# Kernel optimization log

Hardware: AMD Instinct MI355X
Metric: run time of the kernel (lower is better)

## Reference

```python
import jax, jax.numpy as jnp
import numpy as np

B = 4; C = 3; IMG = 256; P = 16; HP = 16; HW = 256
DIM = 512; DEPTH = 6; HEADS = 8; DH = 64
NS = 50; SH = 4; SDH = 64; ITERS = 3; RPD = 128; FF = 2048; N = NS + HW


def _ln(x, g, b):
    m = jnp.mean(x, -1, keepdims=True)
    v = jnp.var(x, -1, keepdims=True)
    return (x - m) * jax.lax.rsqrt(v + 1e-5) * g + b


def _rms(x, g):
    # lucidrains RMSNorm: F.normalize(x, dim=-1) * sqrt(dim) * gamma
    n = jnp.linalg.norm(x, axis=-1, keepdims=True)
    return x / jnp.maximum(n, 1e-12) * (DIM ** 0.5) * g


def setup_inputs() -> dict:
    key = jax.random.key(0)
    ks = iter(jax.random.split(key, 64))
    def W(*s):
        return jax.random.normal(next(ks), s, jnp.float32) * 0.02
    SI = SH * SDH
    d = {}
    d['images'] = jax.random.normal(next(ks), (B, C, IMG, IMG), jnp.float32)
    d['slot_noise'] = jax.random.normal(next(ks), (B, NS, DIM), jnp.float32)
    d['patch_w'] = W(C * P * P, DIM); d['patch_b'] = jnp.zeros((DIM,))
    d['hpos'] = W(HP, DIM); d['wpos'] = W(HP, DIM)
    d['rp_w1'] = W(2, RPD); d['rp_b1'] = jnp.zeros((RPD,))
    d['rp_w2'] = W(RPD, RPD); d['rp_b2'] = jnp.zeros((RPD,))
    d['rp_w3'] = W(RPD, HEADS); d['rp_b3'] = jnp.zeros((HEADS,))
    d['slots_mu'] = W(1, 1, DIM); d['slots_logsigma'] = jnp.zeros((1, 1, DIM))
    d['sa_ln_in_g'] = jnp.ones((DIM,)); d['sa_ln_in_b'] = jnp.zeros((DIM,))
    d['sa_ln_sl_g'] = jnp.ones((DIM,)); d['sa_ln_sl_b'] = jnp.zeros((DIM,))
    d['sa_wq'] = W(DIM, SI); d['sa_bq'] = jnp.zeros((SI,))
    d['sa_wk'] = W(DIM, SI); d['sa_bk'] = jnp.zeros((SI,))
    d['sa_wv'] = W(DIM, SI); d['sa_bv'] = jnp.zeros((SI,))
    d['sa_wo'] = W(SI, DIM); d['sa_bo'] = jnp.zeros((DIM,))
    d['gru_wih'] = W(DIM, 3 * DIM); d['gru_whh'] = W(DIM, 3 * DIM)
    d['gru_bih'] = jnp.zeros((3 * DIM,)); d['gru_bhh'] = jnp.zeros((3 * DIM,))
    d['sa_ln_ff_g'] = jnp.ones((DIM,)); d['sa_ln_ff_b'] = jnp.zeros((DIM,))
    d['sa_mlp_w1'] = W(DIM, DIM); d['sa_mlp_b1'] = jnp.zeros((DIM,))
    d['sa_mlp_w2'] = W(DIM, DIM); d['sa_mlp_b2'] = jnp.zeros((DIM,))
    d['s2c_w'] = W(DIM, 2); d['s2c_b'] = jnp.zeros((2,))
    d['attn_g'] = jnp.ones((DEPTH, DIM))
    d['wq'] = W(DEPTH, DIM, HEADS * DH); d['wk'] = W(DEPTH, DIM, HEADS * DH)
    d['wv'] = W(DEPTH, DIM, HEADS * DH); d['wo'] = W(DEPTH, HEADS * DH, DIM)
    d['ff_g'] = jnp.ones((DEPTH, DIM))
    d['ff_w1'] = W(DEPTH, DIM, FF); d['ff_b1'] = jnp.zeros((DEPTH, FF))
    d['ff_w2'] = W(DEPTH, FF, DIM); d['ff_b2'] = jnp.zeros((DEPTH, DIM))
    d['final_g'] = jnp.ones((DIM,))
    d['pred_w'] = W(DIM, DIM); d['pred_b'] = jnp.zeros((DIM,))
    return d


def reference(images, slot_noise, patch_w, patch_b, hpos, wpos,
              rp_w1, rp_b1, rp_w2, rp_b2, rp_w3, rp_b3,
              slots_mu, slots_logsigma, sa_ln_in_g, sa_ln_in_b, sa_ln_sl_g, sa_ln_sl_b,
              sa_wq, sa_bq, sa_wk, sa_bk, sa_wv, sa_bv, sa_wo, sa_bo,
              gru_wih, gru_whh, gru_bih, gru_bhh, sa_ln_ff_g, sa_ln_ff_b,
              sa_mlp_w1, sa_mlp_b1, sa_mlp_w2, sa_mlp_b2, s2c_w, s2c_b,
              attn_g, wq, wk, wv, wo, ff_g, ff_w1, ff_b1, ff_w2, ff_b2,
              final_g, pred_w, pred_b):
    b = images.shape[0]
    # patchify: b c (h p1) (w p2) -> b h w (p1 p2 c)
    x = images.reshape(b, C, HP, P, HP, P).transpose(0, 2, 4, 3, 5, 1).reshape(b, HP, HP, P * P * C)
    tokens = x @ patch_w + patch_b                     # [b, HP, HP, DIM]
    tokens = tokens + hpos[:, None, :] + wpos[None, :, :]
    tokens = tokens.reshape(b, HW, DIM)
    # --- multi-head slot attention ---
    inp = _ln(tokens, sa_ln_in_g, sa_ln_in_b)
    k = (inp @ sa_wk + sa_bk).reshape(b, HW, SH, SDH).transpose(0, 2, 1, 3)
    v = (inp @ sa_wv + sa_bv).reshape(b, HW, SH, SDH).transpose(0, 2, 1, 3)
    slots = slots_mu + jnp.exp(slots_logsigma) * slot_noise  # [b, NS, DIM]
    scale = SDH ** -0.5
    for _ in range(ITERS):
        prev = slots
        s = _ln(slots, sa_ln_sl_g, sa_ln_sl_b)
        q = (s @ sa_wq + sa_bq).reshape(b, NS, SH, SDH).transpose(0, 2, 1, 3)
        dots = jnp.einsum('bhid,bhjd->bhij', q, k) * scale     # [b, SH, NS, HW]
        attn = jax.nn.softmax(dots, axis=-2) + 1e-8            # softmax over slots
        attn = attn / jnp.sum(attn, -1, keepdims=True)         # weighted mean over inputs
        upd = jnp.einsum('bhij,bhjd->bhid', attn, v)
        upd = upd.transpose(0, 2, 1, 3).reshape(b, NS, SH * SDH) @ sa_wo + sa_bo
        # GRUCell(updates, prev_slots)
        gx = upd @ gru_wih + gru_bih
        gh = prev @ gru_whh + gru_bhh
        xr, xz, xn = jnp.split(gx, 3, -1)
        hr, hz, hn = jnp.split(gh, 3, -1)
        r = jax.nn.sigmoid(xr + hr)
        z = jax.nn.sigmoid(xz + hz)
        nn_ = jnp.tanh(xn + r * hn)
        slots = (1 - z) * nn_ + z * prev
        slots = slots + (jax.nn.relu(_ln(slots, sa_ln_ff_g, sa_ln_ff_b) @ sa_mlp_w1 + sa_mlp_b1) @ sa_mlp_w2 + sa_mlp_b2)
    objects = slots
    slot_coords = objects @ s2c_w + s2c_b              # [b, NS, 2]
    # --- relative position MLP bias (slots coords + patch grid) ---
    g = jnp.arange(HP, dtype=jnp.float32)
    grid = jnp.stack(jnp.meshgrid(g, g, indexing='ij'), -1).reshape(HW, 2)
    coords = jnp.concatenate([slot_coords, jnp.broadcast_to(grid, (b, HW, 2))], axis=1)  # [b, N, 2]
    rel = coords[:, :, None, :] - coords[:, None, :, :]   # [b, N, N, 2]
    hmid = jax.nn.silu(rel @ rp_w1 + rp_b1)
    hmid = jax.nn.silu(hmid @ rp_w2 + rp_b2)
    bias = jnp.transpose(hmid @ rp_w3 + rp_b3, (0, 3, 1, 2))  # [b, HEADS, N, N]
    # --- transformer with per-layer rel-pos bias ---
    x = jnp.concatenate([objects, tokens], axis=1)     # [b, N, DIM]
    ascale = DH ** -0.5
    for l in range(DEPTH):
        h = _rms(x, attn_g[l])
        qh = (h @ wq[l]).reshape(b, N, HEADS, DH).transpose(0, 2, 1, 3)
        kh = (h @ wk[l]).reshape(b, N, HEADS, DH).transpose(0, 2, 1, 3)
        vh = (h @ wv[l]).reshape(b, N, HEADS, DH).transpose(0, 2, 1, 3)
        sim = jnp.einsum('bhid,bhjd->bhij', qh, kh) * ascale + bias
        a = jax.nn.softmax(sim, -1)
        o = jnp.einsum('bhij,bhjd->bhid', a, vh).transpose(0, 2, 1, 3).reshape(b, N, HEADS * DH) @ wo[l]
        x = x + o
        h = _rms(x, ff_g[l])
        x = x + (jax.nn.gelu(h @ ff_w1[l] + ff_b1[l]) @ ff_w2[l] + ff_b2[l])
    x = _rms(x, final_g)
    return x[:, NS:] @ pred_w + pred_b                 # [b, HW, DIM]
```

## Files before the change

### kernel.cpp

```cpp
#include <hip/hip_runtime.h>
#include <hip/hip_bf16.h>

typedef __hip_bfloat16 bf16;
typedef short short8v __attribute__((ext_vector_type(8)));
typedef float float4v __attribute__((ext_vector_type(4)));

static __device__ __forceinline__ float b2f(bf16 x){ return __bfloat162float(x); }

static __device__ __forceinline__ float ldin(const void* p, size_t i, bool isbf) {
  return isbf ? b2f(((const bf16*)p)[i]) : ((const float*)p)[i];
}

static __device__ __forceinline__ unsigned short f2bu(float f) {
  bf16 h = __float2bfloat16(f);
  return *reinterpret_cast<unsigned short*>(&h);
}

#define CDIV(a,b) (((a)+(b)-1)/(b))

#define NB   4
#define NSL  50
#define HWT  256
#define NT   306
#define DIM  512
// ... 104 lines not shown
  for (int k0 = kbeg; k0 < kend; k0 += 32) {
    *(short8v*)&As[srow * LDT + sch] = *(short8v*)ha;
    *(short8v*)&Bs[srow * LDT + sch] = *(short8v*)hb;
    __syncthreads();
    if (k0 + 32 < kend) { fetchA(k0 + 32); fetchB(k0 + 32); }
    short8v a0 = *reinterpret_cast<const short8v*>(&As[(wm + ti)      * LDT + quad * 8]);
    short8v a1 = *reinterpret_cast<const short8v*>(&As[(wm + 16 + ti) * LDT + quad * 8]);
    short8v b0 = *reinterpret_cast<const short8v*>(&Bs[(wn + ti)      * LDT + quad * 8]);
    short8v b1 = *reinterpret_cast<const short8v*>(&Bs[(wn + 16 + ti) * LDT + quad * 8]);
    acc00 = __builtin_amdgcn_mfma_f32_16x16x32_bf16(a0, b0, acc00, 0, 0, 0);
    acc01 = __builtin_amdgcn_mfma_f32_16x16x32_bf16(a0, b1, acc01, 0, 0, 0);
    acc10 = __builtin_amdgcn_mfma_f32_16x16x32_bf16(a1, b0, acc10, 0, 0, 0);
    acc11 = __builtin_amdgcn_mfma_f32_16x16x32_bf16(a1, b1, acc11, 0, 0, 0);
    __syncthreads();
  }

  float4v accs[2][2] = {{acc00, acc01}, {acc10, acc11}};
#pragma unroll
  for (int mi = 0; mi < 2; ++mi) {
#pragma unroll
    for (int ni = 0; ni < 2; ++ni) {
      int row0 = bm + wm + mi * 16 + quad * 4;
      int col  = bn + wn + ni * 16 + ti;
      float bv = (bias && kbeg == 0) ? ldin(bias, boff + col, isbf) : 0.f;
#pragma unroll
      for (int r = 0; r < 4; ++r) {
        int row = row0 + r;
        if (row >= M) continue;
        float v = accs[mi][ni][r] + bv;
        if (act == 1) v = fmaxf(v, 0.f);
        else if (act == 2) {
          float u = 0.7978845608028654f * (v + 0.044715f * v * v * v);
          v = 0.5f * v * (1.f + tanhf(u));
        } else if (act == 3) {
          v = v / (1.f + expf(-v));
        }
        size_t idx = (size_t)row * N + col;
        if (oty) ((bf16*)C)[idx] = __float2bfloat16(v);
        else {
          float* Cf = (float*)C;
          if (mode == 2) atomicAdd(&Cf[idx], v);
          else if (mode == 1) Cf[idx] += v;
          else Cf[idx] = v;
        }
      }
    }
  }
}

__global__ __launch_bounds__(256) void gemm_mfma(
    const void* A, int aty, const unsigned short* WT, size_t woff,
    const void* bias, size_t boff, void* C, int oty,
    int M, int N, int K, int act, int accum, int zsplit, const int* __restrict__ flagp)
{
  int ksz = K / zsplit;
  int kbeg = blockIdx.z * ksz;
  int mode = zsplit > 1 ? 2 : (accum ? 1 : 0);
  gemm_body2(A, aty, WT + woff, bias, boff, C, oty, M, N, K, kbeg, kbeg + ksz,
             act, mode, *flagp != 0);
}

__global__ __launch_bounds__(256) void gemm_mfma_tri(
    const void* A, int aty, const unsigned short* WT, size_t o0, size_t o1, size_t o2,
    void* C0, void* C1, void* C2, int oty, int M, int N, int K,
    const int* __restrict__ flagp)
{
  size_t o = blockIdx.z == 0 ? o0 : (blockIdx.z == 1 ? o1 : o2);
  void* C = blockIdx.z == 0 ? C0 : (blockIdx.z == 1 ? C1 : C2);
  gemm_body2(A, aty, WT + o, nullptr, 0, C, oty, M, N, K, 0, K, 0, 0, *flagp != 0);
}

__global__ __launch_bounds__(256) void gemm_mfma_duo(
    const void* A0, const void* A1, int aty, const unsigned short* WT, size_t o0, size_t o1,
    const void* bias0, const void* bias1, void* C0, void* C1, int oty,
    int M, int N, int K, const int* __restrict__ flagp)
{
  const void* A = blockIdx.z ? A1 : A0;
  size_t o = blockIdx.z ? o1 : o0;
  const void* bias = blockIdx.z ? bias1 : bias0;
  void* C = blockIdx.z ? C1 : C0;
  gemm_body2(A, aty, WT + o, bias, 0, C, oty, M, N, K, 0, K, 0, 0, *flagp != 0);
}

__global__ __launch_bounds__(256) void gemm_k(
    const float* __restrict__ A, const void* __restrict__ W, size_t woff,
    const void* __restrict__ bias, size_t boff, float* __restrict__ C,
    int M, int N, int K, const int* __restrict__ flagp)
{
  const bool isbf = *flagp != 0;
  __shared__ float As[16][68];
  __shared__ float Ws[16][68];
  const int bm = blockIdx.y * 64, bn = blockIdx.x * 64;
  const int tx = threadIdx.x, ty = threadIdx.y;
  const int tid = ty * 16 + tx;
  float acc[4][4] = {};
  for (int k0 = 0; k0 < K; k0 += 16) {
#pragma unroll
    for (int i = 0; i < 4; ++i) {
      int idx = tid + i * 256;
      int m  = idx >> 4, k = idx & 15;
      int gm = bm + m;
      As[k][m] = (gm < M) ? A[(size_t)gm * K + k0 + k] : 0.f;
      int kk = idx >> 6, n = idx & 63;
      int gn = bn + n;
      Ws[kk][n] = (gn < N) ? ldin(W, woff + (size_t)(k0 + kk) * N + gn, isbf) : 0.f;
    }
    __syncthreads();
#pragma unroll
    for (int k = 0; k < 16; ++k) {
      float4 a4 = *reinterpret_cast<const float4*>(&As[k][ty * 4]);
      float4 w4 = *reinterpret_cast<const float4*>(&Ws[k][tx * 4]);
      float a[4] = {a4.x, a4.y, a4.z, a4.w};
      float w[4] = {w4.x, w4.y, w4.z, w4.w};
#pragma unroll
      for (int i = 0; i < 4; ++i)
#pragma unroll
        for (int j = 0; j < 4; ++j)
          acc[i][j] = fmaf(a[i], w[j], acc[i][j]);
    }
    __syncthreads();
  }
#pragma unroll
  for (int i = 0; i < 4; ++i) {
    int gm = bm + ty * 4 + i;
    if (gm >= M) continue;
#pragma unroll
    for (int j = 0; j < 4; ++j) {
      int gn = bn + tx * 4 + j;
      if (gn >= N) continue;
      float v = acc[i][j];
      if (bias) v += ldin(bias, boff + gn, isbf);
      C[(size_t)gm * N + gn] = v;
    }
  }
}

__global__ void patchify_k(const void* __restrict__ img, unsigned short* __restrict__ xp,
                           const int* __restrict__ flagp) {
  const bool isbf = *flagp != 0;
  int i = blockIdx.x * 256 + threadIdx.x;
  if (i >= NB * HWT * 768) return;
  int col = i % 768, row = i / 768;
  int c = col % 3, p2 = (col / 3) & 15, p1 = col / 48;
  int w = row & 15, h = (row >> 4) & 15, b = row >> 8;
  xp[i] = f2bu(ldin(img, (((size_t)(b * 3 + c) * 256 + h * 16 + p1) * 256) + w * 16 + p2, isbf));
}

__global__ void addpos_k(float* __restrict__ tok, const void* __restrict__ hp,
                         const void* __restrict__ wp, const int* __restrict__ flagp) {
  const bool isbf = *flagp != 0;
  int i = blockIdx.x * 256 + threadIdx.x;
  if (i >= NB * HWT * DIM) return;
  int d = i & 511;
  int row = i >> 9;
  int w = row & 15, h = (row >> 4) & 15;
  tok[i] += ldin(hp, h * DIM + d, isbf) + ldin(wp, w * DIM + d, isbf);
}

__global__ void ln512_k(const float* __restrict__ X, const void* __restrict__ g,
                        const void* __restrict__ b, unsigned short* __restrict__ Y,
                        const int* __restrict__ flagp) {
  const bool isbf = *flagp != 0;
  int row = blockIdx.x, t = threadIdx.x;
  const float* x = X + (size_t)row * DIM;
  float v0 = x[t], v1 = x[t + 256];
  __shared__ float rs[256], rq[256];
  rs[t] = v0 + v1; rq[t] = v0 * v0 + v1 * v1;
  __syncthreads();
  for (int o = 128; o > 0; o >>= 1) {
    if (t < o) { rs[t] += rs[t + o]; rq[t] += rq[t + o]; }
    __syncthreads();
  }
  float mean = rs[0] * (1.f / 512.f);
  float var  = rq[0] * (1.f / 512.f) - mean * mean;
  float inv  = rsqrtf(var + 1e-5f);
  unsigned short* y = Y + (size_t)row * DIM;
  y[t]       = f2bu((v0 - mean) * inv * ldin(g, t, isbf)       + ldin(b, t, isbf));
  y[t + 256] = f2bu((v1 - mean) * inv * ldin(g, t + 256, isbf) + ldin(b, t + 256, isbf));
}

__global__ void rms512_k(const float* __restrict__ X, const void* __restrict__ g,
                         int goff, unsigned short* __restrict__ Y, const int* __restrict__ flagp) {
  const bool isbf = *flagp != 0;
  int row = blockIdx.x, t = threadIdx.x;
  const float* x = X + (size_t)row * DIM;
  float v0 = x[t], v1 = x[t + 256];
  __shared__ float rq[256];
  rq[t] = v0 * v0 + v1 * v1;
  __syncthreads();
  for (int o = 128; o > 0; o >>= 1) {
    if (t < o) rq[t] += rq[t + o];
    __syncthreads();
  }
  float nrm = sqrtf(rq[0]);
  float sc = 22.62741699796952f / fmaxf(nrm, 1e-12f);
  unsigned short* y = Y + (size_t)row * DIM;
  y[t]       = f2bu(v0 * sc * ldin(g, goff + t, isbf));
  y[t + 256] = f2bu(v1 * sc * ldin(g, goff + t + 256, isbf));
}

__global__ void slots_init_k(const void* __restrict__ mu, const void* __restrict__ ls,
                             const void* __restrict__ noise, float* __restrict__ slots,
                             const int* __restrict__ flagp) {
  const bool isbf = *flagp != 0;
  int i = blockIdx.x * 256 + threadIdx.x;
  if (i >= NB * NSL * DIM) return;
  int d = i & 511;
  slots[i] = ldin(mu, d, isbf) + expf(ldin(ls, d, isbf)) * ldin(noise, i, isbf);
}

__global__ void slot_dots_k(const float* __restrict__ q, const float* __restrict__ k,
                            float* __restrict__ dots) {
  int blk = blockIdx.x;
  int i = blk % 50, h = (blk / 50) & 3, b = blk / 200;
  int j = threadIdx.x;
  __shared__ float qs[64];
// ... 72 lines not shown
__global__ void relpos_table_k(const void* w1, const void* b1, const void* w2,
                               const void* b2, const void* w3, const void* b3,
                               float* __restrict__ tab, const int* __restrict__ flagp) {
  const bool isbf = *flagp != 0;
  int blk = blockIdx.x;
  float r0 = (float)(blk / 31 - 15), r1 = (float)(blk % 31 - 15);
  int t = threadIdx.x;
  __shared__ float h1[128], h2[128];
  float a = fmaf(r0, ldin(w1, t, isbf), fmaf(r1, ldin(w1, 128 + t, isbf), ldin(b1, t, isbf)));
  h1[t] = a / (1.f + expf(-a));
  __syncthreads();
  float s = ldin(b2, t, isbf);
#pragma unroll 4
  for (int k = 0; k < 128; ++k) s = fmaf(h1[k], ldin(w2, k * 128 + t, isbf), s);
  h2[t] = s / (1.f + expf(-s));
  __syncthreads();
  if (t < 8) {
    float o = ldin(b3, t, isbf);
#pragma unroll 4
    for (int k = 0; k < 128; ++k) o = fmaf(h2[k], ldin(w3, k * 8 + t, isbf), o);
    tab[blk * 8 + t] = o;
  }
}

__global__ void bias_fill_k(const float* __restrict__ tab, float* __restrict__ bias) {
  int i = blockIdx.x * 256 + threadIdx.x;
  if (i >= NB * NH * HWT * HWT) return;
  int jj = i & 255, ii = (i >> 8) & 255, h = (i >> 16) & 7, b = i >> 19;
  int di = (ii >> 4) - (jj >> 4) + 15;
  int dj = (ii & 15) - (jj & 15) + 15;
  bias[(((size_t)(b * NH + h) * NT) + NSL + ii) * NT + NSL + jj] = tab[(di * 31 + dj) * 8 + h];
}

__global__ void rp_l1_k(const float* __restrict__ coords, const void* w1, const void* b1,
                        unsigned short* __restrict__ H, int pbase, int pcount,
                        const int* __restrict__ flagp) {
  const bool isbf = *flagp != 0;
  int idx = blockIdx.x * 256 + threadIdx.x;
  if (idx >= pcount * 128) return;
  int pl = idx >> 7, u = idx & 127;
  int p = pbase + pl;
  int q = p % RPP, bb = p / RPP;
  int ii, jj;
  rp_decode(q, ii, jj);
  float r0 = coords[(bb * NT + ii) * 2]     - coords[(bb * NT + jj) * 2];
  float r1 = coords[(bb * NT + ii) * 2 + 1] - coords[(bb * NT + jj) * 2 + 1];
  float a = fmaf(r0, ldin(w1, u, isbf), fmaf(r1, ldin(w1, 128 + u, isbf), ldin(b1, u, isbf)));
  H[(size_t)pl * 128 + u] = f2bu(a / (1.f + expf(-a)));
}

__global__ __launch_bounds__(256) void rp_l3_k(
    const unsigned short* __restrict__ H2, const void* w3, const void* b3,
    float* __restrict__ bias, int pbase, int pcount, const int* __restrict__ flagp) {
  const bool isbf = *flagp != 0;
  __shared__ float W3s[128 * 8];
  int t = threadIdx.x;
  for (int e = t; e < 1024; e += 256) W3s[e] = ldin(w3, e, isbf);
  __syncthreads();
  int pl = blockIdx.x * 32 + (t >> 3), hh = t & 7;
  if (pl >= pcount) return;
  int p = pbase + pl;
  int q = p % RPP, bb = p / RPP;
  int ii, jj;
  rp_decode(q, ii, jj);
  float s = ldin(b3, hh, isbf);
  const unsigned short* hrow = H2 + (size_t)pl * 128;
#pragma unroll 8
  for (int k = 0; k < 128; ++k) {
    bf16 hv = *reinterpret_cast<const bf16*>(&hrow[k]);
    s = fmaf(b2f(hv), W3s[k * 8 + hh], s);
  }
  bias[((size_t)(bb * NH + hh) * NT + ii) * NT + jj] = s;
}

__global__ void build_x_k(const float* __restrict__ slots, const float* __restrict__ tok,
                          float* __restrict__ x) {
  int i = blockIdx.x * 256 + threadIdx.x;
  if (i >= NB * NT * DIM) return;
  int d = i & 511, n = (i >> 9) % NT, b = i / (NT * DIM);
  x[i] = (n < NSL) ? slots[((size_t)(b * NSL + n)) * DIM + d]
                   : tok[((size_t)(b * HWT + (n - NSL))) * DIM + d];
}

__global__ __launch_bounds__(256) void attn_sim_k(
    const unsigned short* __restrict__ Qb, const unsigned short* __restrict__ Kb,
    const float* __restrict__ bias, float* __restrict__ sim)
{
  const int bh = blockIdx.z, b = bh >> 3, h = bh & 7;
  const int bm = blockIdx.y * 64, bn = blockIdx.x * 64;
  __shared__ unsigned short As[64 * 72];
  __shared__ unsigned short Bs[64 * 72];
  const int tid = threadIdx.x;
  const int lane = tid & 63, wave = tid >> 6, quad = lane >> 4, ti = lane & 15;
  const int wm = (wave & 1) * 32, wn = (wave >> 1) * 32;
  {
    int r = tid >> 2, c = (tid & 3) * 16;
    ushort4 z4 = {0,0,0,0};
    ushort4 a[4] = {z4, z4, z4, z4}, bq[4] = {z4, z4, z4, z4};
    int gi = bm + r, gj = bn + r;
    if (gi < NT) {
      const ushort4* p = reinterpret_cast<const ushort4*>(Qb + ((size_t)(b * NT + gi)) * DIM + h * 64 + c);
#pragma unroll
      for (int i = 0; i < 4; ++i) a[i] = p[i];
    }
    if (gj < NT) {
      const ushort4* p = reinterpret_cast<const ushort4*>(Kb + ((size_t)(b * NT + gj)) * DIM + h * 64 + c);
#pragma unroll
      for (int i = 0; i < 4; ++i) bq[i] = p[i];
    }
#pragma unroll
    for (int i = 0; i < 4; ++i) {
      *reinterpret_cast<ushort4*>(&As[r * 72 + c + i * 4]) = a[i];
      *reinterpret_cast<ushort4*>(&Bs[r * 72 + c + i * 4]) = bq[i];
    }
  }
  __syncthreads();
  float4v acc00 = {0,0,0,0}, acc01 = {0,0,0,0}, acc10 = {0,0,0,0}, acc11 = {0,0,0,0};
#pragma unroll
  for (int ks = 0; ks < 2; ++ks) {
    short8v a0 = *reinterpret_cast<const short8v*>(&As[(wm + ti)      * 72 + ks * 32 + quad * 8]);
    short8v a1 = *reinterpret_cast<const short8v*>(&As[(wm + 16 + ti) * 72 + ks * 32 + quad * 8]);
    short8v b0 = *reinterpret_cast<const short8v*>(&Bs[(wn + ti)      * 72 + ks * 32 + quad * 8]);
    short8v b1 = *reinterpret_cast<const short8v*>(&Bs[(wn + 16 + ti) * 72 + ks * 32 + quad * 8]);
    acc00 = __builtin_amdgcn_mfma_f32_16x16x32_bf16(a0, b0, acc00, 0, 0, 0);
    acc01 = __builtin_amdgcn_mfma_f32_16x16x32_bf16(a0, b1, acc01, 0, 0, 0);
    acc10 = __builtin_amdgcn_mfma_f32_16x16x32_bf16(a1, b0, acc10, 0, 0, 0);
    acc11 = __builtin_amdgcn_mfma_f32_16x16x32_bf16(a1, b1, acc11, 0, 0, 0);
  }
  float4v accs[2][2] = {{acc00, acc01}, {acc10, acc11}};
#pragma unroll
  for (int mi = 0; mi < 2; ++mi) {
#pragma unroll
    for (int ni = 0; ni < 2; ++ni) {
      int row0 = bm + wm + mi * 16 + quad * 4;
      int col  = bn + wn + ni * 16 + ti;
      if (col >= NT) continue;
#pragma unroll
      for (int r = 0; r < 4; ++r) {
        int row = row0 + r;
        if (row >= NT) continue;
        size_t idx = ((size_t)bh * NT + row) * NT + col;
        sim[idx] = accs[mi][ni][r] * 0.125f + bias[idx];
      }
    }
  }
}

__global__ void softmax_prob_k(const float* __restrict__ sim, unsigned short* __restrict__ prob) {
  int row = blockIdx.x;
  const float* src = sim + (size_t)row * NT;
  unsigned short* dst = prob + (size_t)row * 320;
  int t = threadIdx.x;
  float v0 = (t < NT) ? src[t] : -1e30f;
  float v1 = (t + 256 < NT) ? src[t + 256] : -1e30f;
  __shared__ float rb[256];
  rb[t] = fmaxf(v0, v1);
  __syncthreads();
  for (int o = 128; o > 0; o >>= 1) {
    if (t < o) rb[t] = fmaxf(rb[t], rb[t + o]);
    __syncthreads();
  }
  float m = rb[0];
  __syncthreads();
  float e0 = (t < NT) ? expf(v0 - m) : 0.f;
  float e1 = (t + 256 < NT) ? expf(v1 - m) : 0.f;
  rb[t] = e0 + e1;
  __syncthreads();
  for (int o = 128; o > 0; o >>= 1) {
    if (t < o) rb[t] += rb[t + o];
    __syncthreads();
  }
  float inv = 1.f / rb[0];
  dst[t] = f2bu(e0 * inv);
  if (t + 256 < 320) dst[t + 256] = f2bu(t + 256 < NT ? e1 * inv : 0.f);
}

__global__ __launch_bounds__(256) void attn_av_k(
    const unsigned short* __restrict__ prob, const unsigned short* __restrict__ Vb,
    unsigned short* __restrict__ Ob)
{
  const int bh = blockIdx.y, b = bh >> 3, h = bh & 7;
  const int bm = blockIdx.x * 64;
  __shared__ unsigned short As[64 * LDT];
  __shared__ unsigned short Bs[64 * LDT];
  const int tid = threadIdx.x;
  const int lane = tid & 63, wave = tid >> 6, quad = lane >> 4, ti = lane & 15;
  const int wm = (wave & 1) * 32, wn = (wave >> 1) * 32;
  const int arow = tid >> 2, ach = (tid & 3) * 8;
  const int bk = tid & 31, bch = tid >> 5;

  float4v acc00 = {0,0,0,0}, acc01 = {0,0,0,0}, acc10 = {0,0,0,0}, acc11 = {0,0,0,0};

  for (int k0 = 0; k0 < 320; k0 += 32) {
    {
      int gi = bm + arow;
      ushort4 u0 = {0,0,0,0}, u1 = {0,0,0,0};
      if (gi < NT) {
        const ushort4* p = reinterpret_cast<const ushort4*>(
            prob + ((size_t)bh * NT + gi) * 320 + k0 + ach);
        u0 = p[0]; u1 = p[1];
      }
      *reinterpret_cast<ushort4*>(&As[arow * LDT + ach])     = u0;
      *reinterpret_cast<ushort4*>(&As[arow * LDT + ach + 4]) = u1;
    }
    {
      int j = k0 + bk;
      unsigned short h8[8];
      if (j < NT) {
        const ushort4* p = reinterpret_cast<const ushort4*>(
            Vb + ((size_t)(b * NT + j)) * DIM + h * 64 + bch * 8);
        ushort4 u0 = p[0], u1 = p[1];
        h8[0]=u0.x; h8[1]=u0.y; h8[2]=u0.z; h8[3]=u0.w; h8[4]=u1.x; h8[5]=u1.y; h8[6]=u1.z; h8[7]=u1.w;
      } else {
#pragma unroll
        for (int i = 0; i < 8; ++i) h8[i] = 0;
      }
#pragma unroll
      for (int i = 0; i < 8; ++i) Bs[(bch * 8 + i) * LDT + bk] = h8[i];
    }
    __syncthreads();
    short8v a0 = *reinterpret_cast<const short8v*>(&As[(wm + ti)      * LDT + quad * 8]);
    short8v a1 = *reinterpret_cast<const short8v*>(&As[(wm + 16 + ti) * LDT + quad * 8]);
    short8v b0 = *reinterpret_cast<const short8v*>(&Bs[(wn + ti)      * LDT + quad * 8]);
    short8v b1 = *reinterpret_cast<const short8v*>(&Bs[(wn + 16 + ti) * LDT + quad * 8]);
    acc00 = __builtin_amdgcn_mfma_f32_16x16x32_bf16(a0, b0, acc00, 0, 0, 0);
    acc01 = __builtin_amdgcn_mfma_f32_16x16x32_bf16(a0, b1, acc01, 0, 0, 0);
    acc10 = __builtin_amdgcn_mfma_f32_16x16x32_bf16(a1, b0, acc10, 0, 0, 0);
    acc11 = __builtin_amdgcn_mfma_f32_16x16x32_bf16(a1, b1, acc11, 0, 0, 0);
    __syncthreads();
  }
  float4v accs[2][2] = {{acc00, acc01}, {acc10, acc11}};
#pragma unroll
  for (int mi = 0; mi < 2; ++mi) {
#pragma unroll
    for (int ni = 0; ni < 2; ++ni) {
      int row0 = bm + wm + mi * 16 + quad * 4;
      int col  = wn + ni * 16 + ti;
#pragma unroll
      for (int r = 0; r < 4; ++r) {
        int row = row0 + r;
        if (row >= NT) continue;
        Ob[((size_t)(b * NT + row)) * DIM + h * 64 + col] = f2bu(accs[mi][ni][r]);
      }
    }
  }
}

__global__ void write_out_k(const float* __restrict__ tmp, void* __restrict__ out,
                            const int* __restrict__ flagp) {
  const bool isbf = *flagp != 0;
  int i = blockIdx.x * 256 + threadIdx.x;
  if (i >= NB * HWT * DIM) return;
  int d = i & 511, tt = (i >> 9) & 255, b = i / (HWT * DIM);
  float v = tmp[((size_t)(b * NT + NSL + tt)) * DIM + d];
  if (isbf) ((bf16*)out)[i] = __float2bfloat16(v);
  else      ((float*)out)[i] = v;
}

extern "C" void kernel_launch(void* const* d_in, const int* in_sizes, int n_in,
                              void* d_out, int out_size, void* d_ws, size_t ws_size,
                              hipStream_t stream) {
  const void* images        = d_in[0];
  const void* slot_noise    = d_in[1];
  const void* patch_w       = d_in[2];
  const void* patch_b       = d_in[3];
  const void* hpos          = d_in[4];
  const void* wpos          = d_in[5];
  const void* rp_w1         = d_in[6];
  const void* rp_b1         = d_in[7];
  const void* rp_w2         = d_in[8];
  const void* rp_b2         = d_in[9];
  const void* rp_w3         = d_in[10];
  const void* rp_b3         = d_in[11];
  const void* slots_mu      = d_in[12];
  const void* slots_logsig  = d_in[13];
  const void* sa_ln_in_g    = d_in[14];
  const void* sa_ln_in_b    = d_in[15];
  const void* sa_ln_sl_g    = d_in[16];
  const void* sa_ln_sl_b    = d_in[17];
  const void* sa_wq         = d_in[18];
  const void* sa_bq         = d_in[19];
  const void* sa_wk         = d_in[20];
  const void* sa_bk         = d_in[21];
  const void* sa_wv         = d_in[22];
  const void* sa_bv         = d_in[23];
  const void* sa_wo         = d_in[24];
  const void* sa_bo         = d_in[25];
  const void* gru_wih       = d_in[26];
  const void* gru_whh       = d_in[27];
  const void* gru_bih       = d_in[28];
  const void* gru_bhh       = d_in[29];
  const void* sa_ln_ff_g    = d_in[30];
  const void* sa_ln_ff_b    = d_in[31];
  const void* sa_mlp_w1     = d_in[32];
  const void* sa_mlp_b1     = d_in[33];
  const void* sa_mlp_w2     = d_in[34];
  const void* sa_mlp_b2     = d_in[35];
  const void* s2c_w         = d_in[36];
  const void* s2c_b         = d_in[37];
  const void* attn_g        = d_in[38];
  const void* wq            = d_in[39];
  const void* wk            = d_in[40];
  const void* wv            = d_in[41];
  const void* wo            = d_in[42];
  const void* ff_g          = d_in[43];
  const void* ff_w1         = d_in[44];
  const void* ff_b1         = d_in[45];
  const void* ff_w2         = d_in[46];
  const void* ff_b2         = d_in[47];
  const void* final_g       = d_in[48];
  const void* pred_w        = d_in[49];
  const void* pred_b        = d_in[50];

  float* ws = (float*)d_ws;
  int* FLAG = (int*)ws;
  size_t off = 16;
  auto alloc = [&](size_t n) { float* p = ws + off; off += (n + 15) & ~(size_t)15; return p; };
  float* TOK   = alloc((size_t)NB * HWT * DIM);
  unsigned short* INPB = (unsigned short*)alloc((size_t)NB * HWT * DIM / 2);
  float* KB    = alloc((size_t)NB * HWT * 256);
  float* VB    = alloc((size_t)NB * HWT * 256);
  float* SLOTS = alloc((size_t)NB * NSL * DIM);
  unsigned short* SLNB = (unsigned short*)alloc((size_t)NB * NSL * DIM / 2);
  float* QB    = alloc((size_t)NB * NSL * 256);
  float* ATT   = alloc((size_t)NB * 4 * NSL * HWT);
  float* UPD   = alloc((size_t)NB * NSL * 256);
  float* UPDP  = alloc((size_t)NB * NSL * DIM);
  unsigned short* HIDSB = (unsigned short*)alloc((size_t)NB * NSL * DIM / 2);
  float* SC    = alloc((size_t)NB * NSL * 2);
  float* CRD   = alloc((size_t)NB * NT * 2);
  float* TAB   = alloc((size_t)961 * 8);
  float* BIAS  = alloc((size_t)NB * NH * NT * NT);
  float* X     = alloc((size_t)NB * NT * DIM);
  unsigned short* HBB  = (unsigned short*)alloc((size_t)NB * NT * DIM / 2);
  unsigned short* QHB  = (unsigned short*)alloc((size_t)NB * NT * DIM / 2);
  unsigned short* KHB  = (unsigned short*)alloc((size_t)NB * NT * DIM / 2);
  unsigned short* VHB  = (unsigned short*)alloc((size_t)NB * NT * DIM / 2);
  float* SIM   = alloc((size_t)NB * NH * NT * NT);
  unsigned short* PROBB = (unsigned short*)alloc((size_t)NB * NH * NT * 320 / 2);
  unsigned short* OBB  = (unsigned short*)alloc((size_t)NB * NT * DIM / 2);
  unsigned short* FFHB = (unsigned short*)alloc((size_t)NB * NT * FF / 2);
  float* OUTT  = alloc((size_t)NB * NT * DIM);
  unsigned short* XPB = (unsigned short*)OUTT;
  float* GX = SIM;
  float* GH = SIM + (size_t)NB * NSL * 1536;
  const size_t oPatch = 0;
  const size_t oKw    = oPatch + (size_t)512 * 768;
  const size_t oVw    = oKw    + (size_t)256 * 512;
  const size_t oQw    = oVw    + (size_t)256 * 512;
  const size_t oWo    = oQw    + (size_t)256 * 512;
  const size_t oGih   = oWo    + (size_t)512 * 256;
  const size_t oGhh   = oGih   + (size_t)1536 * 512;
  const size_t oMlp1  = oGhh   + (size_t)1536 * 512;
  const size_t oMlp2  = oMlp1  + (size_t)512 * 512;
  const size_t oRp2   = oMlp2  + (size_t)512 * 512;
  const size_t oWq    = oRp2   + (size_t)128 * 128;
  const size_t oWk    = oWq    + (size_t)6 * 512 * 512;
  const size_t oWv    = oWk    + (size_t)6 * 512 * 512;
  const size_t oWol   = oWv    + (size_t)6 * 512 * 512;
  const size_t oFf1   = oWol   + (size_t)6 * 512 * 512;
  const size_t oFf2   = oFf1   + (size_t)6 * 512 * 2048;
  const size_t oPred  = oFf2   + (size_t)6 * 2048 * 512;
  const size_t wtTotal = oPred + (size_t)512 * 512;
  unsigned short* WTS = (unsigned short*)alloc((wtTotal + 1) / 2);
  (void)ws_size; (void)in_sizes; (void)n_in; (void)out_size;

#define GEMMM(A_, ATY_, WOFF_, BIAS_, BOFF_, C_, OTY_, M_, N_, K_, ACT_, ACC_, ZS_) \
  gemm_mfma<<<dim3((N_)/64, CDIV((M_),64), (ZS_)), 256, 0, stream>>>( \
      A_, ATY_, WTS, (size_t)(WOFF_), BIAS_, (size_t)(BOFF_), C_, OTY_, M_, N_, K_, ACT_, ACC_, ZS_, FLAG)

  const int MROW = NB * NT;
  const int MS   = NB * NSL;

  detect_k<<<1, 256, 0, stream>>>(images, FLAG);
  wtrans_k<<<dim3(8, 12, 1),  256, 0, stream>>>(patch_w,  WTS + oPatch, 768,  512,  FLAG);
  wtrans_k<<<dim3(4, 8, 1),   256, 0, stream>>>(sa_wk,    WTS + oKw,    512,  256,  FLAG);
  wtrans_k<<<dim3(4, 8, 1),   256, 0, stream>>>(sa_wv,    WTS + oVw,    512,  256,  FLAG);
  wtrans_k<<<dim3(4, 8, 1),   256, 0, stream>>>(sa_wq,    WTS + oQw,    512,  256,  FLAG);
  wtrans_k<<<dim3(8, 4, 1),   256, 0, stream>>>(sa_wo,    WTS + oWo,    256,  512,  FLAG);
  wtrans_k<<<dim3(24, 8, 1),  256, 0, stream>>>(gru_wih,  WTS + oGih,   512,  1536, FLAG);
  wtrans_k<<<dim3(24, 8, 1),  256, 0, stream>>>(gru_whh,  WTS + oGhh,   512,  1536, FLAG);
  wtrans_k<<<dim3(8, 8, 1),   256, 0, stream>>>(sa_mlp_w1, WTS + oMlp1, 512,  512,  FLAG);
  wtrans_k<<<dim3(8, 8, 1),   256, 0, stream>>>(sa_mlp_w2, WTS + oMlp2, 512,  512,  FLAG);
  wtrans_k<<<dim3(2, 2, 1),   256, 0, stream>>>(rp_w2,    WTS + oRp2,   128,  128,  FLAG);
  wtrans_k<<<dim3(8, 8, 6),   256, 0, stream>>>(wq,       WTS + oWq,    512,  512,  FLAG);
  wtrans_k<<<dim3(8, 8, 6),   256, 0, stream>>>(wk,       WTS + oWk,    512,  512,  FLAG);
  wtrans_k<<<dim3(8, 8, 6),   256, 0, stream>>>(wv,       WTS + oWv,    512,  512,  FLAG);
  wtrans_k<<<dim3(8, 8, 6),   256, 0, stream>>>(wo,       WTS + oWol,   512,  512,  FLAG);
  wtrans_k<<<dim3(32, 8, 6),  256, 0, stream>>>(ff_w1,    WTS + oFf1,   512,  2048, FLAG);
  wtrans_k<<<dim3(8, 32, 6),  256, 0, stream>>>(ff_w2,    WTS + oFf2,   2048, 512,  FLAG);
  wtrans_k<<<dim3(8, 8, 1),   256, 0, stream>>>(pred_w,   WTS + oPred,  512,  512,  FLAG);

  patchify_k<<<CDIV(NB*HWT*768, 256), 256, 0, stream>>>(images, XPB, FLAG);
  hipMemsetAsync(TOK, 0, (size_t)NB * HWT * DIM * sizeof(float), stream);
  GEMMM(XPB, 1, oPatch, patch_b, 0, TOK, 0, NB*HWT, DIM, 768, 0, 0, 3);
  addpos_k<<<CDIV(NB*HWT*DIM, 256), 256, 0, stream>>>(TOK, hpos, wpos, FLAG);

  ln512_k<<<NB*HWT, 256, 0, stream>>>(TOK, sa_ln_in_g, sa_ln_in_b, INPB, FLAG);
  gemm_mfma_duo<<<dim3(4, 16, 2), 256, 0, stream>>>(
      INPB, INPB, 1, WTS, oKw, oVw, sa_bk, sa_bv, KB, VB, 0, NB*HWT, 256, DIM, FLAG);
  slots_init_k<<<CDIV(NB*NSL*DIM, 256), 256, 0, stream>>>(slots_mu, slots_logsig, slot_noise, SLOTS, FLAG);

  for (int it = 0; it < 3; ++it) {
    ln512_k<<<MS, 256, 0, stream>>>(SLOTS, sa_ln_sl_g, sa_ln_sl_b, SLNB, FLAG);
    GEMMM(SLNB, 1, oQw, sa_bq, 0, QB, 0, MS, 256, DIM, 0, 0, 1);
    slot_dots_k<<<NB*4*NSL, 256, 0, stream>>>(QB, KB, ATT);
    softmax_slots_k<<<16, 256, 0, stream>>>(ATT);
    renorm_attn_k<<<NB*4*NSL, 256, 0, stream>>>(ATT);
    slot_upd_k<<<MS, 256, 0, stream>>>(ATT, VB, UPD);
    GEMMM(UPD, 0, oWo, sa_bo, 0, UPDP, 0, MS, DIM, 256, 0, 0, 1);
    gemm_mfma_duo<<<dim3(24, 4, 2), 256, 0, stream>>>(
        UPDP, SLOTS, 0, WTS, oGih, oGhh, gru_bih, gru_bhh, GX, GH, 0, MS, 1536, DIM, FLAG);
    gru_k<<<CDIV(NB*NSL*DIM, 256), 256, 0, stream>>>(GX, GH, SLOTS);
    ln512_k<<<MS, 256, 0, stream>>>(SLOTS, sa_ln_ff_g, sa_ln_ff_b, SLNB, FLAG);
    GEMMM(SLNB, 1, oMlp1, sa_mlp_b1, 0, HIDSB, 1, MS, DIM, DIM, 1, 0, 1);
    GEMMM(HIDSB, 1, oMlp2, sa_mlp_b2, 0, SLOTS, 0, MS, DIM, DIM, 0, 1, 1);
  }

  gemm_k<<<dim3(1, CDIV(MS,64)), dim3(16,16), 0, stream>>>(
      SLOTS, s2c_w, 0, s2c_b, 0, SC, MS, 2, DIM, FLAG);
  build_coords_k<<<CDIV(NB*NT, 256), 256, 0, stream>>>(SC, CRD);
  relpos_table_k<<<961, 128, 0, stream>>>(rp_w1, rp_b1, rp_w2, rp_b2, rp_w3, rp_b3, TAB, FLAG);
  bias_fill_k<<<CDIV(NB*NH*HWT*HWT, 256), 256, 0, stream>>>(TAB, BIAS);
  {
    unsigned short* H1 = HBB;
    unsigned short* H2 = HBB + (size_t)PCH * 128;
    for (int c = 0; c < 2; ++c) {
      int pb = c * PCH;
      rp_l1_k<<<CDIV(PCH*128, 256), 256, 0, stream>>>(CRD, rp_w1, rp_b1, H1, pb, PCH, FLAG);
      GEMMM(H1, 1, oRp2, rp_b2, 0, H2, 1, PCH, 128, 128, 3, 0, 1);
      rp_l3_k<<<CDIV(PCH,32), 256, 0, stream>>>(H2, rp_w3, rp_b3, BIAS, pb, PCH, FLAG);
    }
  }

  build_x_k<<<CDIV(NB*NT*DIM, 256), 256, 0, stream>>>(SLOTS, TOK, X);
  for (int l = 0; l < 6; ++l) {
    size_t lw = (size_t)l * 512 * 512;
    rms512_k<<<MROW, 256, 0, stream>>>(X, attn_g, l * DIM, HBB, FLAG);
    gemm_mfma_tri<<<dim3(8, 20, 3), 256, 0, stream>>>(
        HBB, 1, WTS, oWq + lw, oWk + lw, oWv + lw, QHB, KHB, VHB, 1, MROW, DIM, DIM, FLAG);
    attn_sim_k<<<dim3(CDIV(NT,64), CDIV(NT,64), NB*NH), 256, 0, stream>>>(QHB, KHB, BIAS, SIM);
    softmax_prob_k<<<NB*NH*NT, 256, 0, stream>>>(SIM, PROBB);
    attn_av_k<<<dim3(CDIV(NT,64), NB*NH), 256, 0, stream>>>(PROBB, VHB, OBB);
    GEMMM(OBB, 1, oWol + lw, (const void*)nullptr, 0, X, 0, MROW, DIM, DIM, 0, 1, 2);
    rms512_k<<<MROW, 256, 0, stream>>>(X, ff_g, l * DIM, HBB, FLAG);
    GEMMM(HBB, 1, oFf1 + (size_t)l * 512 * 2048, ff_b1, l * FF, FFHB, 1, MROW, FF, DIM, 2, 0, 1);
    GEMMM(FFHB, 1, oFf2 + (size_t)l * 2048 * 512, ff_b2, l * DIM, X, 0, MROW, DIM, FF, 0, 1, 4);
  }

  rms512_k<<<MROW, 256, 0, stream>>>(X, final_g, 0, HBB, FLAG);
  hipMemsetAsync(OUTT, 0, (size_t)NB * NT * DIM * sizeof(float), stream);
  GEMMM(HBB, 1, oPred, pred_b, 0, OUTT, 0, MROW, DIM, DIM, 0, 0, 2);
  write_out_k<<<CDIV(NB*HWT*DIM, 256), 256, 0, stream>>>(OUTT, d_out, FLAG);

#undef GEMMM
}
```

Measured before the change: 1.408 ms.

## Fuse attention scores, softmax and AV into one kernel; add s2c reduction kernel

Replaces the three-kernel attention path (score GEMM writing fp32 sim, row softmax writing bf16 probabilities, AV GEMM) with one kernel per 32-query tile. Each tile keeps the full score row in shared memory, applies the bias and softmax, then multiplies by V staged transposed in LDS. This removes the global round-trips for the sim and prob buffers and two launches per layer, at the cost of about 48KB of LDS per block and only 320 blocks. It also swaps the generic fp32 tiled GEMM used for the N=2 slot-to-coord projection for a per-row dot-product reduction kernel.

```diff
diff --git a/kernel.cpp b/kernel.cpp
--- a/kernel.cpp
+++ b/kernel.cpp
@@ -210,56 +210,25 @@
   gemm_body2(A, aty, WT + o, bias, 0, C, oty, M, N, K, 0, K, 0, 0, *flagp != 0);
 }
 
-__global__ __launch_bounds__(256) void gemm_k(
-    const float* __restrict__ A, const void* __restrict__ W, size_t woff,
-    const void* __restrict__ bias, size_t boff, float* __restrict__ C,
-    int M, int N, int K, const int* __restrict__ flagp)
-{
-  const bool isbf = *flagp != 0;
-  __shared__ float As[16][68];
-  __shared__ float Ws[16][68];
-  const int bm = blockIdx.y * 64, bn = blockIdx.x * 64;
-  const int tx = threadIdx.x, ty = threadIdx.y;
-  const int tid = ty * 16 + tx;
-  float acc[4][4] = {};
-  for (int k0 = 0; k0 < K; k0 += 16) {
-#pragma unroll
-    for (int i = 0; i < 4; ++i) {
-      int idx = tid + i * 256;
-      int m  = idx >> 4, k = idx & 15;
-      int gm = bm + m;
-      As[k][m] = (gm < M) ? A[(size_t)gm * K + k0 + k] : 0.f;
-      int kk = idx >> 6, n = idx & 63;
-      int gn = bn + n;
-      Ws[kk][n] = (gn < N) ? ldin(W, woff + (size_t)(k0 + kk) * N + gn, isbf) : 0.f;
-    }
-    __syncthreads();
-#pragma unroll
-    for (int k = 0; k < 16; ++k) {
-      float4 a4 = *reinterpret_cast<const float4*>(&As[k][ty * 4]);
-      float4 w4 = *reinterpret_cast<const float4*>(&Ws[k][tx * 4]);
-      float a[4] = {a4.x, a4.y, a4.z, a4.w};
-      float w[4] = {w4.x, w4.y, w4.z, w4.w};
-#pragma unroll
-      for (int i = 0; i < 4; ++i)
-#pragma unroll
-        for (int j = 0; j < 4; ++j)
-          acc[i][j] = fmaf(a[i], w[j], acc[i][j]);
-    }
-    __syncthreads();
-  }
-#pragma unroll
-  for (int i = 0; i < 4; ++i) {
-    int gm = bm + ty * 4 + i;
-    if (gm >= M) continue;
-#pragma unroll
-    for (int j = 0; j < 4; ++j) {
-      int gn = bn + tx * 4 + j;
-      if (gn >= N) continue;
-      float v = acc[i][j];
-      if (bias) v += ldin(bias, boff + gn, isbf);
-      C[(size_t)gm * N + gn] = v;
-    }
+__global__ void s2c_k(const float* __restrict__ slots, const void* __restrict__ w,
+                      const void* __restrict__ bv, float* __restrict__ sc,
+                      const int* __restrict__ flagp) {
+  const bool isbf = *flagp != 0;
+  int row = blockIdx.x, t = threadIdx.x;
+  const float* x = slots + (size_t)row * DIM;
+  float v0 = x[t], v1 = x[t + 256];
+  float a0 = v0 * ldin(w, 2 * t, isbf)     + v1 * ldin(w, 2 * (t + 256), isbf);
+  float a1 = v0 * ldin(w, 2 * t + 1, isbf) + v1 * ldin(w, 2 * (t + 256) + 1, isbf);
+  __shared__ float r0[256], r1[256];
+  r0[t] = a0; r1[t] = a1;
+  __syncthreads();
+  for (int o = 128; o > 0; o >>= 1) {
+    if (t < o) { r0[t] += r0[t + o]; r1[t] += r1[t + o]; }
+    __syncthreads();
+  }
+  if (t == 0) {
+    sc[row * 2]     = r0[0] + ldin(bv, 0, isbf);
+    sc[row * 2 + 1] = r1[0] + ldin(bv, 1, isbf);
   }
 }
 
@@ -498,166 +467,140 @@
                    : tok[((size_t)(b * HWT + (n - NSL))) * DIM + d];
 }
 
-__global__ __launch_bounds__(256) void attn_sim_k(
+__global__ __launch_bounds__(256) void attn_fused_k(
     const unsigned short* __restrict__ Qb, const unsigned short* __restrict__ Kb,
-    const float* __restrict__ bias, float* __restrict__ sim)
-{
-  const int bh = blockIdx.z, b = bh >> 3, h = bh & 7;
-  const int bm = blockIdx.y * 64, bn = blockIdx.x * 64;
-  __shared__ unsigned short As[64 * 72];
-  __shared__ unsigned short Bs[64 * 72];
-  const int tid = threadIdx.x;
-  const int lane = tid & 63, wave = tid >> 6, quad = lane >> 4, ti = lane & 15;
-  const int wm = (wave & 1) * 32, wn = (wave >> 1) * 32;
-  {
-    int r = tid >> 2, c = (tid & 3) * 16;
-    ushort4 z4 = {0,0,0,0};
-    ushort4 a[4] = {z4, z4, z4, z4}, bq[4] = {z4, z4, z4, z4};
-    int gi = bm + r, gj = bn + r;
-    if (gi < NT) {
-      const ushort4* p = reinterpret_cast<const ushort4*>(Qb + ((size_t)(b * NT + gi)) * DIM + h * 64 + c);
-#pragma unroll
-      for (int i = 0; i < 4; ++i) a[i] = p[i];
-    }
-    if (gj < NT) {
-      const ushort4* p = reinterpret_cast<const ushort4*>(Kb + ((size_t)(b * NT + gj)) * DIM + h * 64 + c);
-#pragma unroll
-      for (int i = 0; i < 4; ++i) bq[i] = p[i];
-    }
-#pragma unroll
-    for (int i = 0; i < 4; ++i) {
-      *reinterpret_cast<ushort4*>(&As[r * 72 + c + i * 4]) = a[i];
-      *reinterpret_cast<ushort4*>(&Bs[r * 72 + c + i * 4]) = bq[i];
-    }
-  }
-  __syncthreads();
-  float4v acc00 = {0,0,0,0}, acc01 = {0,0,0,0}, acc10 = {0,0,0,0}, acc11 = {0,0,0,0};
-#pragma unroll
-  for (int ks = 0; ks < 2; ++ks) {
-    short8v a0 = *reinterpret_cast<const short8v*>(&As[(wm + ti)      * 72 + ks * 32 + quad * 8]);
-    short8v a1 = *reinterpret_cast<const short8v*>(&As[(wm + 16 + ti) * 72 + ks * 32 + quad * 8]);
-    short8v b0 = *reinterpret_cast<const short8v*>(&Bs[(wn + ti)      * 72 + ks * 32 + quad * 8]);
-    short8v b1 = *reinterpret_cast<const short8v*>(&Bs[(wn + 16 + ti) * 72 + ks * 32 + quad * 8]);
-    acc00 = __builtin_amdgcn_mfma_f32_16x16x32_bf16(a0, b0, acc00, 0, 0, 0);
-    acc01 = __builtin_amdgcn_mfma_f32_16x16x32_bf16(a0, b1, acc01, 0, 0, 0);
-    acc10 = __builtin_amdgcn_mfma_f32_16x16x32_bf16(a1, b0, acc10, 0, 0, 0);
-    acc11 = __builtin_amdgcn_mfma_f32_16x16x32_bf16(a1, b1, acc11, 0, 0, 0);
-  }
-  float4v accs[2][2] = {{acc00, acc01}, {acc10, acc11}};
-#pragma unroll
-  for (int mi = 0; mi < 2; ++mi) {
-#pragma unroll
-    for (int ni = 0; ni < 2; ++ni) {
-      int row0 = bm + wm + mi * 16 + quad * 4;
-      int col  = bn + wn + ni * 16 + ti;
-      if (col >= NT) continue;
-#pragma unroll
-      for (int r = 0; r < 4; ++r) {
-        int row = row0 + r;
-        if (row >= NT) continue;
-        size_t idx = ((size_t)bh * NT + row) * NT + col;
-        sim[idx] = accs[mi][ni][r] * 0.125f + bias[idx];
-      }
-    }
-  }
-}
-
-__global__ void softmax_prob_k(const float* __restrict__ sim, unsigned short* __restrict__ prob) {
-  int row = blockIdx.x;
-  const float* src = sim + (size_t)row * NT;
-  unsigned short* dst = prob + (size_t)row * 320;
-  int t = threadIdx.x;
-  float v0 = (t < NT) ? src[t] : -1e30f;
-  float v1 = (t + 256 < NT) ? src[t + 256] : -1e30f;
-  __shared__ float rb[256];
-  rb[t] = fmaxf(v0, v1);
-  __syncthreads();
-  for (int o = 128; o > 0; o >>= 1) {
-    if (t < o) rb[t] = fmaxf(rb[t], rb[t + o]);
-    __syncthreads();
-  }
-  float m = rb[0];
-  __syncthreads();
-  float e0 = (t < NT) ? expf(v0 - m) : 0.f;
-  float e1 = (t + 256 < NT) ? expf(v1 - m) : 0.f;
-  rb[t] = e0 + e1;
-  __syncthreads();
-  for (int o = 128; o > 0; o >>= 1) {
-    if (t < o) rb[t] += rb[t + o];
-    __syncthreads();
-  }
-  float inv = 1.f / rb[0];
-  dst[t] = f2bu(e0 * inv);
-  if (t + 256 < 320) dst[t + 256] = f2bu(t + 256 < NT ? e1 * inv : 0.f);
-}
-
-__global__ __launch_bounds__(256) void attn_av_k(
-    const unsigned short* __restrict__ prob, const unsigned short* __restrict__ Vb,
+    const unsigned short* __restrict__ Vb, const float* __restrict__ bias,
     unsigned short* __restrict__ Ob)
 {
   const int bh = blockIdx.y, b = bh >> 3, h = bh & 7;
-  const int bm = blockIdx.x * 64;
-  __shared__ unsigned short As[64 * LDT];
-  __shared__ unsigned short Bs[64 * LDT];
+  const int i0 = blockIdx.x * 32;
+  __shared__ unsigned short Qs[32 * 72];
+  __shared__ unsigned short Ks[64 * 72];
+  __shared__ float S[32 * 332];
+  unsigned short* P = (unsigned short*)S;
+
   const int tid = threadIdx.x;
   const int lane = tid & 63, wave = tid >> 6, quad = lane >> 4, ti = lane & 15;
-  const int wm = (wave & 1) * 32, wn = (wave >> 1) * 32;
-  const int arow = tid >> 2, ach = (tid & 3) * 8;
-  const int bk = tid & 31, bch = tid >> 5;
-
-  float4v acc00 = {0,0,0,0}, acc01 = {0,0,0,0}, acc10 = {0,0,0,0}, acc11 = {0,0,0,0};
-
-  for (int k0 = 0; k0 < 320; k0 += 32) {
+  const int mi = wave & 1, nh = wave >> 1;
+
+  {
+    int r = tid >> 3, c = (tid & 7) * 8;
+    int gi = i0 + r;
+    ushort4 u0 = {0,0,0,0}, u1 = {0,0,0,0};
+    if (gi < NT) {
+      const ushort4* p = (const ushort4*)(Qb + ((size_t)(b * NT + gi)) * DIM + h * 64 + c);
+      u0 = p[0]; u1 = p[1];
+    }
+    *(ushort4*)&Qs[r * 72 + c] = u0;
+    *(ushort4*)&Qs[r * 72 + c + 4] = u1;
+  }
+
+  for (int kt = 0; kt < 5; ++kt) {
+    __syncthreads();
     {
-      int gi = bm + arow;
-      ushort4 u0 = {0,0,0,0}, u1 = {0,0,0,0};
-      if (gi < NT) {
-        const ushort4* p = reinterpret_cast<const ushort4*>(
-            prob + ((size_t)bh * NT + gi) * 320 + k0 + ach);
-        u0 = p[0]; u1 = p[1];
+      int kr = tid >> 2, c = (tid & 3) * 16;
+      int gj = kt * 64 + kr;
+      ushort4 v[4] = {{0,0,0,0},{0,0,0,0},{0,0,0,0},{0,0,0,0}};
+      if (gj < NT) {
+        const ushort4* p = (const ushort4*)(Kb + ((size_t)(b * NT + gj)) * DIM + h * 64 + c);
+#pragma unroll
+        for (int i = 0; i < 4; ++i) v[i] = p[i];
       }
-      *reinterpret_cast<ushort4*>(&As[arow * LDT + ach])     = u0;
-      *reinterpret_cast<ushort4*>(&As[arow * LDT + ach + 4]) = u1;
-    }
+#pragma unroll
+      for (int i = 0; i < 4; ++i) *(ushort4*)&Ks[kr * 72 + c + i * 4] = v[i];
+    }
+    __syncthreads();
+#pragma unroll
+    for (int ntl = 0; ntl < 2; ++ntl) {
+      int nt = nh * 2 + ntl;
+      float4v acc = {0,0,0,0};
+#pragma unroll
+      for (int ks = 0; ks < 2; ++ks) {
+        short8v a  = *(const short8v*)&Qs[(mi * 16 + ti) * 72 + ks * 32 + quad * 8];
+        short8v bb = *(const short8v*)&Ks[(nt * 16 + ti) * 72 + ks * 32 + quad * 8];
+        acc = __builtin_amdgcn_mfma_f32_16x16x32_bf16(a, bb, acc, 0, 0, 0);
+      }
+      int colL = kt * 64 + nt * 16 + ti;
+      int row0 = mi * 16 + quad * 4;
+#pragma unroll
+      for (int r = 0; r < 4; ++r) {
+        int row_g = i0 + row0 + r;
+        float val;
+        if (colL < NT) {
+          float bv = (row_g < NT) ? bias[((size_t)bh * NT + row_g) * NT + colL] : 0.f;
+          val = acc[r] * 0.125f + bv;
+        } else val = -1e30f;
+        S[(row0 + r) * 332 + colL] = val;
+      }
+    }
+  }
+  __syncthreads();
+
+  {
+    int rl = tid >> 3, sub = tid & 7;
+    float sv[40];
+#pragma unroll
+    for (int k = 0; k < 40; ++k) sv[k] = S[rl * 332 + sub + k * 8];
+    float m = -1e30f;
+#pragma unroll
+    for (int k = 0; k < 40; ++k) m = fmaxf(m, sv[k]);
+    m = fmaxf(m, __shfl_xor(m, 1));
+    m = fmaxf(m, __shfl_xor(m, 2));
+    m = fmaxf(m, __shfl_xor(m, 4));
+    float s = 0.f;
+#pragma unroll
+    for (int k = 0; k < 40; ++k) { float e = __expf(sv[k] - m); sv[k] = e; s += e; }
+    s += __shfl_xor(s, 1);
+    s += __shfl_xor(s, 2);
+    s += __shfl_xor(s, 4);
+    float inv = 1.f / s;
+    __syncthreads();
+#pragma unroll
+    for (int k = 0; k < 40; ++k) P[rl * 664 + sub + k * 8] = f2bu(sv[k] * inv);
+  }
+
+  float4v oacc[2] = {{0,0,0,0},{0,0,0,0}};
+  for (int vt = 0; vt < 5; ++vt) {
+    __syncthreads();
     {
-      int j = k0 + bk;
-      unsigned short h8[8];
-      if (j < NT) {
-        const ushort4* p = reinterpret_cast<const ushort4*>(
-            Vb + ((size_t)(b * NT + j)) * DIM + h * 64 + bch * 8);
-        ushort4 u0 = p[0], u1 = p[1];
-        h8[0]=u0.x; h8[1]=u0.y; h8[2]=u0.z; h8[3]=u0.w; h8[4]=u1.x; h8[5]=u1.y; h8[6]=u1.z; h8[7]=u1.w;
+      int key = tid & 63, d0 = (tid >> 6) * 16;
+      int gj = vt * 64 + key;
+      unsigned short hv[16];
+      if (gj < NT) {
+        const ushort4* p = (const ushort4*)(Vb + ((size_t)(b * NT + gj)) * DIM + h * 64 + d0);
+#pragma unroll
+        for (int i = 0; i < 4; ++i) {
+          ushort4 u = p[i];
+          hv[i*4+0]=u.x; hv[i*4+1]=u.y; hv[i*4+2]=u.z; hv[i*4+3]=u.w;
+        }
       } else {
 #pragma unroll
-        for (int i = 0; i < 8; ++i) h8[i] = 0;
+        for (int i = 0; i < 16; ++i) hv[i] = 0;
       }
 #pragma unroll
-      for (int i = 0; i < 8; ++i) Bs[(bch * 8 + i) * LDT + bk] = h8[i];
-    }
-    __syncthreads();
-    short8v a0 = *reinterpret_cast<const short8v*>(&As[(wm + ti)      * LDT + quad * 8]);
-    short8v a1 = *reinterpret_cast<const short8v*>(&As[(wm + 16 + ti) * LDT + quad * 8]);
-    short8v b0 = *reinterpret_cast<const short8v*>(&Bs[(wn + ti)      * LDT + quad * 8]);
-    short8v b1 = *reinterpret_cast<const short8v*>(&Bs[(wn + 16 + ti) * LDT + quad * 8]);
-    acc00 = __builtin_amdgcn_mfma_f32_16x16x32_bf16(a0, b0, acc00, 0, 0, 0);
-    acc01 = __builtin_amdgcn_mfma_f32_16x16x32_bf16(a0, b1, acc01, 0, 0, 0);
-    acc10 = __builtin_amdgcn_mfma_f32_16x16x32_bf16(a1, b0, acc10, 0, 0, 0);
-    acc11 = __builtin_amdgcn_mfma_f32_16x16x32_bf16(a1, b1, acc11, 0, 0, 0);
-    __syncthreads();
-  }
-  float4v accs[2][2] = {{acc00, acc01}, {acc10, acc11}};
-#pragma unroll
-  for (int mi = 0; mi < 2; ++mi) {
-#pragma unroll
-    for (int ni = 0; ni < 2; ++ni) {
-      int row0 = bm + wm + mi * 16 + quad * 4;
-      int col  = wn + ni * 16 + ti;
-#pragma unroll
-      for (int r = 0; r < 4; ++r) {
-        int row = row0 + r;
-        if (row >= NT) continue;
-        Ob[((size_t)(b * NT + row)) * DIM + h * 64 + col] = f2bu(accs[mi][ni][r]);
+      for (int i = 0; i < 16; ++i) Ks[(d0 + i) * 72 + key] = hv[i];
+    }
+    __syncthreads();
+#pragma unroll
+    for (int ntl = 0; ntl < 2; ++ntl) {
+      int nt = nh * 2 + ntl;
+#pragma unroll
+      for (int ks = 0; ks < 2; ++ks) {
+        short8v a  = *(const short8v*)&P[(mi * 16 + ti) * 664 + vt * 64 + ks * 32 + quad * 8];
+        short8v bb = *(const short8v*)&Ks[(nt * 16 + ti) * 72 + ks * 32 + quad * 8];
+        oacc[ntl] = __builtin_amdgcn_mfma_f32_16x16x32_bf16(a, bb, oacc[ntl], 0, 0, 0);
       }
+    }
+  }
+
+#pragma unroll
+  for (int ntl = 0; ntl < 2; ++ntl) {
+    int dim = nh * 32 + ntl * 16 + ti;
+#pragma unroll
+    for (int r = 0; r < 4; ++r) {
+      int row_g = i0 + mi * 16 + quad * 4 + r;
+      if (row_g < NT)
+        Ob[((size_t)(b * NT + row_g)) * DIM + h * 64 + dim] = f2bu(oacc[ntl][r]);
     }
   }
 }
@@ -757,6 +700,7 @@
   unsigned short* OBB  = (unsigned short*)alloc((size_t)NB * NT * DIM / 2);
   unsigned short* FFHB = (unsigned short*)alloc((size_t)NB * NT * FF / 2);
   float* OUTT  = alloc((size_t)NB * NT * DIM);
+  (void)PROBB;
   unsigned short* XPB = (unsigned short*)OUTT;
   float* GX = SIM;
   float* GH = SIM + (size_t)NB * NSL * 1536;
@@ -833,8 +777,7 @@
     GEMMM(HIDSB, 1, oMlp2, sa_mlp_b2, 0, SLOTS, 0, MS, DIM, DIM, 0, 1, 1);
   }
 
-  gemm_k<<<dim3(1, CDIV(MS,64)), dim3(16,16), 0, stream>>>(
-      SLOTS, s2c_w, 0, s2c_b, 0, SC, MS, 2, DIM, FLAG);
+  s2c_k<<<MS, 256, 0, stream>>>(SLOTS, s2c_w, s2c_b, SC, FLAG);
   build_coords_k<<<CDIV(NB*NT, 256), 256, 0, stream>>>(SC, CRD);
   relpos_table_k<<<961, 128, 0, stream>>>(rp_w1, rp_b1, rp_w2, rp_b2, rp_w3, rp_b3, TAB, FLAG);
   bias_fill_k<<<CDIV(NB*NH*HWT*HWT, 256), 256, 0, stream>>>(TAB, BIAS);
@@ -855,9 +798,7 @@
     rms512_k<<<MROW, 256, 0, stream>>>(X, attn_g, l * DIM, HBB, FLAG);
     gemm_mfma_tri<<<dim3(8, 20, 3), 256, 0, stream>>>(
         HBB, 1, WTS, oWq + lw, oWk + lw, oWv + lw, QHB, KHB, VHB, 1, MROW, DIM, DIM, FLAG);
-    attn_sim_k<<<dim3(CDIV(NT,64), CDIV(NT,64), NB*NH), 256, 0, stream>>>(QHB, KHB, BIAS, SIM);
-    softmax_prob_k<<<NB*NH*NT, 256, 0, stream>>>(SIM, PROBB);
-    attn_av_k<<<dim3(CDIV(NT,64), NB*NH), 256, 0, stream>>>(PROBB, VHB, OBB);
+    attn_fused_k<<<dim3(10, NB*NH), 256, 0, stream>>>(QHB, KHB, VHB, BIAS, OBB);
     GEMMM(OBB, 1, oWol + lw, (const void*)nullptr, 0, X, 0, MROW, DIM, DIM, 0, 1, 2);
     rms512_k<<<MROW, 256, 0, stream>>>(X, ff_g, l * DIM, HBB, FLAG);
     GEMMM(HBB, 1, oFf1 + (size_t)l * 512 * 2048, ff_b1, l * FF, FFHB, 1, MROW, FF, DIM, 2, 0, 1);
```

Result: faster. 1.310 ms (-7.0%).
